# Performance work log

Measured on AMD Instinct MI355X. Metric: run time of the kernel, lower is better.

## Reference

```python
import jax, jax.numpy as jnp
import numpy as np

N_NODES = 100000
N_EDGES = 1600000
IN_DIM, HID_DIM, OUT_DIM = 128, 64, 64


def setup_inputs() -> dict:
    key = jax.random.key(0)
    ks = jax.random.split(key, 6)
    feat = jax.random.normal(ks[0], (N_NODES, IN_DIM), dtype=jnp.float32)
    W1 = jax.random.normal(ks[1], (IN_DIM, HID_DIM), dtype=jnp.float32) * (IN_DIM ** -0.5)
    W2 = jax.random.normal(ks[2], (HID_DIM, HID_DIM), dtype=jnp.float32) * (HID_DIM ** -0.5)
    W3 = jax.random.normal(ks[3], (HID_DIM, OUT_DIM), dtype=jnp.float32) * (HID_DIM ** -0.5)
    b1 = jnp.zeros((HID_DIM,), jnp.float32)
    b2 = jnp.zeros((HID_DIM,), jnp.float32)
    b3 = jnp.zeros((OUT_DIM,), jnp.float32)
    src = jax.random.randint(ks[4], (N_EDGES,), 0, N_NODES, dtype=jnp.int32)
    dst = jax.random.randint(ks[5], (N_EDGES,), 0, N_NODES, dtype=jnp.int32)
    return {"feat": feat, "W1": W1, "b1": b1, "W2": W2, "b2": b2,
            "W3": W3, "b3": b3, "src": src, "dst": dst}


def _degree_norms(src, dst, n_nodes):
    ones = jnp.ones(src.shape[0], jnp.float32)
    out_deg = jax.ops.segment_sum(ones, src, num_segments=n_nodes)
    in_deg = jax.ops.segment_sum(ones, dst, num_segments=n_nodes)
    # DGL GraphConv norm='both': D_out^{-1/2} on source side, D_in^{-1/2} on dest side
    norm_src = jnp.clip(out_deg, 1.0, None) ** -0.5
    norm_dst = jnp.clip(in_deg, 1.0, None) ** -0.5
    return norm_src, norm_dst


def _graph_conv(h, W, b, src, dst, norm_src, norm_dst, n_nodes):
    # mult-first (in_dim >= out_dim path of DGL; linear so mathematically equivalent)
    hw = (h * norm_src[:, None]) @ W          # [N, out]
    msgs = hw[src]                             # [E, out] gather
    agg = jax.ops.segment_sum(msgs, dst, num_segments=n_nodes)  # [N, out] scatter-add
    return agg * norm_dst[:, None] + b


def reference(feat, W1, b1, W2, b2, W3, b3, src, dst):
    n_nodes = feat.shape[0]
    norm_src, norm_dst = _degree_norms(src, dst, n_nodes)
    h = feat
    for W, b in ((W1, b1), (W2, b2), (W3, b3)):
        h = _graph_conv(h, W, b, src, dst, norm_src, norm_dst, n_nodes)
        h = jax.nn.relu(h)
    return h
```

## Files before the change

### kernel.cpp

```cpp
#include <hip/hip_runtime.h>
#include <hip/hip_fp16.h>
#include <type_traits>

#define N_NODES 100000
#define N_EDGES 1600000
#define NB 391
#define CHUNKS 128
#define EPB (N_EDGES / CHUNKS)
#define HALF_NODES 50000
#define WORDS_HALF 12500
#define WORDS_ALL 25000

__global__ void __launch_bounds__(256) hist_kernel(const int* __restrict__ src,
                                                   const int* __restrict__ dst,
                                                   unsigned* __restrict__ histA,
                                                   unsigned* __restrict__ histB) {
    __shared__ unsigned h[WORDS_HALF];
    const int b   = blockIdx.x;
    const int dir = b >> 8;
    const int r   = (b >> 7) & 1;
    const int c   = b & 127;
    const int* __restrict__ ids = dir ? dst : src;
    unsigned* __restrict__ hist = dir ? histB : histA;
    for (int i = threadIdx.x; i < WORDS_HALF; i += 256) h[i] = 0u;
    __syncthreads();
    const int base = c * EPB;
    const int lo   = r * HALF_NODES;
    for (int e = base + threadIdx.x; e < base + EPB; e += 256) {
        int id = ids[e] - lo;
        if ((unsigned)id < (unsigned)HALF_NODES)
            atomicAdd(&h[id >> 2], 1u << ((id & 3) * 8));
    }
    __syncthreads();
    unsigned* __restrict__ out = hist + c * WORDS_ALL + r * WORDS_HALF;
    for (int i = threadIdx.x; i < WORDS_HALF; i += 256) out[i] = h[i];
}

__global__ void reduce_src_kernel(const unsigned* __restrict__ histA,
                                  float* __restrict__ norm_src) {
    const int w = blockIdx.x * 256 + threadIdx.x;
    if (w >= WORDS_ALL) return;
    unsigned s0 = 0, s1 = 0, s2 = 0, s3 = 0;
#pragma unroll 4
    for (int c = 0; c < CHUNKS; ++c) {
        unsigned v = histA[c * WORDS_ALL + w];
        s0 += v & 255u;
        s1 += (v >> 8) & 255u;
        s2 += (v >> 16) & 255u;
        s3 += v >> 24;
    }
    const int n = w * 4;
    norm_src[n + 0] = rsqrtf((float)(s0 > 1u ? s0 : 1u));
    norm_src[n + 1] = rsqrtf((float)(s1 > 1u ? s1 : 1u));
    norm_src[n + 2] = rsqrtf((float)(s2 > 1u ? s2 : 1u));
    norm_src[n + 3] = rsqrtf((float)(s3 > 1u ? s3 : 1u));
}

__global__ void scan_dst_kernel(unsigned* __restrict__ histB,
                                unsigned* __restrict__ ideg,
                                float* __restrict__ norm_dst) {
    const int w = blockIdx.x * 256 + threadIdx.x;
    if (w >= WORDS_ALL) return;
    unsigned run = 0;
#pragma unroll 4
    for (int c = 0; c < CHUNKS; ++c) {
        unsigned v = histB[c * WORDS_ALL + w];
        histB[c * WORDS_ALL + w] = run;
        run += v;
    }
    unsigned s0 = run & 255u, s1 = (run >> 8) & 255u, s2 = (run >> 16) & 255u, s3 = run >> 24;
    const int n = w * 4;
    ideg[n + 0] = s0; ideg[n + 1] = s1; ideg[n + 2] = s2; ideg[n + 3] = s3;
    norm_dst[n + 0] = rsqrtf((float)(s0 > 1u ? s0 : 1u));
    norm_dst[n + 1] = rsqrtf((float)(s1 > 1u ? s1 : 1u));
    norm_dst[n + 2] = rsqrtf((float)(s2 > 1u ? s2 : 1u));
    norm_dst[n + 3] = rsqrtf((float)(s3 > 1u ? s3 : 1u));
}

__global__ void partial_sum_kernel(const unsigned* __restrict__ ideg, int* __restrict__ blocksum) {
    __shared__ int s[256];
    int i = blockIdx.x * 256 + threadIdx.x;
    int c = (i < N_NODES) ? (int)ideg[i] : 0;
    s[threadIdx.x] = c;
    __syncthreads();
    for (int off = 128; off > 0; off >>= 1) {
        if (threadIdx.x < off) s[threadIdx.x] += s[threadIdx.x + off];
        __syncthreads();
    }
    if (threadIdx.x == 0) blocksum[blockIdx.x] = s[0];
}

__global__ void scan_sums_kernel(const int* __restrict__ blocksum, int* __restrict__ blockoff,
                                 int* __restrict__ row_start) {
    __shared__ int s[512];
    const int t = threadIdx.x;
    int v0 = (t < NB) ? blocksum[t] : 0;
    s[t] = v0;
    __syncthreads();
    for (int off = 1; off < 512; off <<= 1) {
        int v = (t >= off) ? s[t - off] : 0;
        __syncthreads();
        s[t] += v;
        __syncthreads();
    }
    if (t < NB) blockoff[t] = s[t] - v0;
    if (t == 0) row_start[N_NODES] = N_EDGES;
}

__global__ void write_offsets_kernel(const unsigned* __restrict__ ideg, const int* __restrict__ blockoff,
                                     int* __restrict__ row_start) {
    __shared__ int s[256];
    const int t = threadIdx.x;
    const int i = blockIdx.x * 256 + t;
    int c = (i < N_NODES) ? (int)ideg[i] : 0;
    s[t] = c;
    __syncthreads();
    for (int off = 1; off < 256; off <<= 1) {
        int v = (t >= off) ? s[t - off] : 0;
        __syncthreads();
        s[t] += v;
        __syncthreads();
    }
    if (i < N_NODES) row_start[i] = blockoff[blockIdx.x] + s[t] - c;
}

__global__ void __launch_bounds__(256) scatter_kernel(const int* __restrict__ src,
                                                      const int* __restrict__ dst,
                                                      const unsigned* __restrict__ histB,
                                                      const int* __restrict__ row_start,
                                                      int* __restrict__ sorted_src) {
    __shared__ unsigned cur[WORDS_HALF];
    const int c = blockIdx.x;
    const int r = blockIdx.y;
    const unsigned* __restrict__ pref = histB + c * WORDS_ALL + r * WORDS_HALF;
    for (int i = threadIdx.x; i < WORDS_HALF; i += 256) cur[i] = pref[i];
    __syncthreads();
    const int base = c * EPB;
    const int lo   = r * HALF_NODES;
    for (int e = base + threadIdx.x; e < base + EPB; e += 256) {
        int d  = dst[e];
        int dl = d - lo;
        if ((unsigned)dl < (unsigned)HALF_NODES) {
            unsigned old = atomicAdd(&cur[dl >> 2], 1u << ((dl & 3) * 8));
            unsigned rk  = (old >> ((dl & 3) * 8)) & 255u;
            sorted_src[row_start[d] + (int)rk] = src[e];
        }
    }
}

template <int K, typename IN>
__global__ void __launch_bounds__(256) gemm_kernel(const IN* __restrict__ h,
                                                   const float* __restrict__ W,
                                                   const float* __restrict__ norm_src,
                                                   __half* __restrict__ out) {
    __shared__ float Ws[K * 64];
    __shared__ float hs[64][68];
    const int t  = threadIdx.x;
    const int ty = t >> 4;
    const int tx = t & 15;
    const int nb = blockIdx.x * 64;

#pragma unroll
    for (int i = 0; i < K * 16 / 256; ++i)
        ((float4*)Ws)[i * 256 + t] = ((const float4*)W)[i * 256 + t];

    float a[4][4];
#pragma unroll
    for (int m = 0; m < 4; ++m)
#pragma unroll
        for (int j = 0; j < 4; ++j) a[m][j] = 0.f;

    for (int kk = 0; kk < K; kk += 64) {
        __syncthreads();
        if constexpr (std::is_same<IN, float>::value) {
#pragma unroll
            for (int r = 0; r < 4; ++r) {
                int e = r * 1024 + t * 4;
                int m = e >> 6, k = e & 63;
                int node = nb + m;
                float4 v = make_float4(0.f, 0.f, 0.f, 0.f);
                if (node < N_NODES) v = *(const float4*)&h[(size_t)node * K + kk + k];
                *(float4*)&hs[m][k] = v;
            }
        } else {
#pragma unroll
            for (int r = 0; r < 2; ++r) {
                int e = r * 2048 + t * 8;
                int m = e >> 6, k = e & 63;
                int node = nb + m;
                float4 lo = make_float4(0.f, 0.f, 0.f, 0.f);
                float4 hi = make_float4(0.f, 0.f, 0.f, 0.f);
                if (node < N_NODES) {
                    uint4 raw = *reinterpret_cast<const uint4*>(&h[(size_t)node * K + kk + k]);
                    float2 f0 = __half22float2(*reinterpret_cast<__half2*>(&raw.x));
                    float2 f1 = __half22float2(*reinterpret_cast<__half2*>(&raw.y));
                    float2 f2 = __half22float2(*reinterpret_cast<__half2*>(&raw.z));
                    float2 f3 = __half22float2(*reinterpret_cast<__half2*>(&raw.w));
                    lo = make_float4(f0.x, f0.y, f1.x, f1.y);
                    hi = make_float4(f2.x, f2.y, f3.x, f3.y);
                }
                *(float4*)&hs[m][k]     = lo;
                *(float4*)&hs[m][k + 4] = hi;
            }
        }
        __syncthreads();

#pragma unroll 4
        for (int k = 0; k < 64; k += 4) {
            float w[4][4], hr[4][4];
#pragma unroll
            for (int i = 0; i < 4; ++i) {
                float4 wv = *(const float4*)&Ws[(kk + k + i) * 64 + tx * 4];
                w[i][0] = wv.x; w[i][1] = wv.y; w[i][2] = wv.z; w[i][3] = wv.w;
            }
#pragma unroll
            for (int m = 0; m < 4; ++m) {
                float4 hv = *(const float4*)&hs[ty * 4 + m][k];
                hr[m][0] = hv.x; hr[m][1] = hv.y; hr[m][2] = hv.z; hr[m][3] = hv.w;
            }
#pragma unroll
            for (int m = 0; m < 4; ++m)
#pragma unroll
                for (int i = 0; i < 4; ++i)
#pragma unroll
                    for (int j = 0; j < 4; ++j)
                        a[m][j] = fmaf(hr[m][i], w[i][j], a[m][j]);
        }
    }

#pragma unroll
    for (int m = 0; m < 4; ++m) {
        int node = nb + ty * 4 + m;
        if (node < N_NODES) {
            float ns = norm_src[node];
            __half2 p0 = __floats2half2_rn(a[m][0] * ns, a[m][1] * ns);
            __half2 p1 = __floats2half2_rn(a[m][2] * ns, a[m][3] * ns);
            uint2 raw;
            raw.x = *reinterpret_cast<unsigned*>(&p0);
            raw.y = *reinterpret_cast<unsigned*>(&p1);
            *reinterpret_cast<uint2*>(&out[(size_t)node * 64 + tx * 4]) = raw;
        }
    }
}

template <typename OUT>
__global__ void __launch_bounds__(256) agg_kernel(const __half* __restrict__ hw,
                                                  const int* __restrict__ sorted_src,
                                                  const int* __restrict__ row_start,
                                                  const float* __restrict__ norm_dst,
                                                  const float* __restrict__ b,
                                                  OUT* __restrict__ out) {
    const int node = blockIdx.x * 4 + (threadIdx.x >> 6);
    const int lane = threadIdx.x & 63;
    const int g    = lane >> 3;
    const int q    = lane & 7;
    const int beg = row_start[node];
    const int end = row_start[node + 1];

    float a0[8], a1[8], a2[8], a3[8];
#pragma unroll
    for (int j = 0; j < 8; ++j) { a0[j] = 0.f; a1[j] = 0.f; a2[j] = 0.f; a3[j] = 0.f; }

#define GCN_GATHER(acc, idx)                                                                  \
    do {                                                                                      \
        uint4 raw = *reinterpret_cast<const uint4*>(&hw[(size_t)sorted_src[idx] * 64 + q * 8]); \
        float2 f0 = __half22float2(*reinterpret_cast<__half2*>(&raw.x));                      \
        float2 f1 = __half22float2(*reinterpret_cast<__half2*>(&raw.y));                      \
        float2 f2 = __half22float2(*reinterpret_cast<__half2*>(&raw.z));                      \
        float2 f3 = __half22float2(*reinterpret_cast<__half2*>(&raw.w));                      \
        acc[0] += f0.x; acc[1] += f0.y; acc[2] += f1.x; acc[3] += f1.y;                       \
        acc[4] += f2.x; acc[5] += f2.y; acc[6] += f3.x; acc[7] += f3.y;                       \
    } while (0)

    for (int e = beg + g; e < end; e += 32) {
        int i0 = e, i1 = e + 8, i2 = e + 16, i3 = e + 24;
        if (i0 < end) GCN_GATHER(a0, i0);
        if (i1 < end) GCN_GATHER(a1, i1);
        if (i2 < end) GCN_GATHER(a2, i2);
        if (i3 < end) GCN_GATHER(a3, i3);
    }
#undef GCN_GATHER

#pragma unroll
    for (int j = 0; j < 8; ++j) a0[j] += a1[j] + a2[j] + a3[j];

#pragma unroll
    for (int j = 0; j < 8; ++j) {
        a0[j] += __shfl_xor(a0[j], 8);
        a0[j] += __shfl_xor(a0[j], 16);
        a0[j] += __shfl_xor(a0[j], 32);
    }

    if (g == 0) {
        float ns = norm_dst[node];
        float o[8];
#pragma unroll
        for (int j = 0; j < 8; ++j) {
            float v = fmaf(a0[j], ns, b[q * 8 + j]);
            o[j] = v > 0.f ? v : 0.f;
        }
        if constexpr (std::is_same<OUT, float>::value) {
            *(float4*)&out[(size_t)node * 64 + q * 8]     = make_float4(o[0], o[1], o[2], o[3]);
            *(float4*)&out[(size_t)node * 64 + q * 8 + 4] = make_float4(o[4], o[5], o[6], o[7]);
        } else {
            __half2 p0 = __floats2half2_rn(o[0], o[1]);
            __half2 p1 = __floats2half2_rn(o[2], o[3]);
            __half2 p2 = __floats2half2_rn(o[4], o[5]);
            __half2 p3 = __floats2half2_rn(o[6], o[7]);
            uint4 raw;
            raw.x = *reinterpret_cast<unsigned*>(&p0);
            raw.y = *reinterpret_cast<unsigned*>(&p1);
            raw.z = *reinterpret_cast<unsigned*>(&p2);
            raw.w = *reinterpret_cast<unsigned*>(&p3);
            *reinterpret_cast<uint4*>(&out[(size_t)node * 64 + q * 8]) = raw;
        }
    }
}

extern "C" void kernel_launch(void* const* d_in, const int* in_sizes, int n_in,
                              void* d_out, int out_size, void* d_ws, size_t ws_size,
                              hipStream_t stream) {
    const float* feat = (const float*)d_in[0];
    const float* W1   = (const float*)d_in[1];
    const float* b1   = (const float*)d_in[2];
    const float* W2   = (const float*)d_in[3];
    const float* b2   = (const float*)d_in[4];
    const float* W3   = (const float*)d_in[5];
    const float* b3   = (const float*)d_in[6];
    const int*   src  = (const int*)d_in[7];
    const int*   dst  = (const int*)d_in[8];
    float* out = (float*)d_out;

    char* ws = (char*)d_ws;
    size_t off = 0;
    auto alloc = [&](size_t bytes) { char* p = ws + off; off += (bytes + 255) & ~size_t(255); return p; };
    float*    norm_src   = (float*)alloc(N_NODES * 4);
    float*    norm_dst   = (float*)alloc(N_NODES * 4);
    unsigned* ideg       = (unsigned*)alloc(N_NODES * 4);
    int*      row_start  = (int*)alloc((N_NODES + 1) * 4);
    int*      blocksum   = (int*)alloc(NB * 4);
    int*      blockoff   = (int*)alloc(NB * 4);
    int*      sorted_src = (int*)alloc(N_EDGES * 4);
    __half*   hw         = (__half*)alloc(N_NODES * 64 * 2);
    __half*   hb         = (__half*)alloc(N_NODES * 64 * 2);

    unsigned* histA = (unsigned*)hw;
    unsigned* histB = (unsigned*)hb;

    hist_kernel<<<512, 256, 0, stream>>>(src, dst, histA, histB);
    reduce_src_kernel<<<98, 256, 0, stream>>>(histA, norm_src);
    scan_dst_kernel<<<98, 256, 0, stream>>>(histB, ideg, norm_dst);

    partial_sum_kernel<<<NB, 256, 0, stream>>>(ideg, blocksum);
    scan_sums_kernel<<<1, 512, 0, stream>>>(blocksum, blockoff, row_start);
    write_offsets_kernel<<<NB, 256, 0, stream>>>(ideg, blockoff, row_start);

    scatter_kernel<<<dim3(128, 2), 256, 0, stream>>>(src, dst, histB, row_start, sorted_src);

    const int GEMM_GRID = (N_NODES + 63) / 64;
    const int AGG_GRID  = (N_NODES + 3) / 4;

    gemm_kernel<128, float><<<GEMM_GRID, 256, 0, stream>>>(feat, W1, norm_src, hw);
    agg_kernel<__half><<<AGG_GRID, 256, 0, stream>>>(hw, sorted_src, row_start, norm_dst, b1, hb);

    gemm_kernel<64, __half><<<GEMM_GRID, 256, 0, stream>>>(hb, W2, norm_src, hw);
    agg_kernel<__half><<<AGG_GRID, 256, 0, stream>>>(hw, sorted_src, row_start, norm_dst, b2, hb);

    gemm_kernel<64, __half><<<GEMM_GRID, 256, 0, stream>>>(hb, W3, norm_src, hw);
    agg_kernel<float><<<AGG_GRID, 256, 0, stream>>>(hw, sorted_src, row_start, norm_dst, b3, out);
}
```

Baseline: 381.8 us.

## Fuse degree/partial-sum kernels, vectorise offsets, and use half-wave per node in aggregation

Merges the source-degree reduction, destination scan and block partial sums into one kernel, shrinking the block-sum scan to 98 blocks. Offsets and histogram init/copy are vectorised to 4 words per thread. The aggregation kernel now assigns 32 lanes per node instead of 64 with a single accumulator set, which should raise lane utilisation at the average degree of 16. In exchange, each group carries less memory-level parallelism per lane.

```diff
diff --git a/kernel.cpp b/kernel.cpp
--- a/kernel.cpp
+++ b/kernel.cpp
@@ -4,25 +4,27 @@
 
 #define N_NODES 100000
 #define N_EDGES 1600000
-#define NB 391
 #define CHUNKS 128
 #define EPB (N_EDGES / CHUNKS)
 #define HALF_NODES 50000
 #define WORDS_HALF 12500
 #define WORDS_ALL 25000
+#define VEC_HALF 3125
+#define NBB 98
 
 __global__ void __launch_bounds__(256) hist_kernel(const int* __restrict__ src,
                                                    const int* __restrict__ dst,
                                                    unsigned* __restrict__ histA,
                                                    unsigned* __restrict__ histB) {
-    __shared__ unsigned h[WORDS_HALF];
+    __shared__ __align__(16) unsigned h[WORDS_HALF];
     const int b   = blockIdx.x;
     const int dir = b >> 8;
     const int r   = (b >> 7) & 1;
     const int c   = b & 127;
     const int* __restrict__ ids = dir ? dst : src;
     unsigned* __restrict__ hist = dir ? histB : histA;
-    for (int i = threadIdx.x; i < WORDS_HALF; i += 256) h[i] = 0u;
+    for (int i = threadIdx.x; i < VEC_HALF; i += 256)
+        ((uint4*)h)[i] = make_uint4(0u, 0u, 0u, 0u);
     __syncthreads();
     const int base = c * EPB;
     const int lo   = r * HALF_NODES;
@@ -32,88 +34,91 @@
             atomicAdd(&h[id >> 2], 1u << ((id & 3) * 8));
     }
     __syncthreads();
-    unsigned* __restrict__ out = hist + c * WORDS_ALL + r * WORDS_HALF;
-    for (int i = threadIdx.x; i < WORDS_HALF; i += 256) out[i] = h[i];
-}
-
-__global__ void reduce_src_kernel(const unsigned* __restrict__ histA,
-                                  float* __restrict__ norm_src) {
-    const int w = blockIdx.x * 256 + threadIdx.x;
-    if (w >= WORDS_ALL) return;
-    unsigned s0 = 0, s1 = 0, s2 = 0, s3 = 0;
+    unsigned* __restrict__ outp = hist + c * WORDS_ALL + r * WORDS_HALF;
+    for (int i = threadIdx.x; i < VEC_HALF; i += 256)
+        ((uint4*)outp)[i] = ((const uint4*)h)[i];
+}
+
+__global__ void __launch_bounds__(256) degrees_kernel(const unsigned* __restrict__ histA,
+                                                      unsigned* __restrict__ histB,
+                                                      float* __restrict__ norm_src,
+                                                      unsigned* __restrict__ ideg,
+                                                      float* __restrict__ norm_dst,
+                                                      int* __restrict__ blocksum) {
+    __shared__ int sred[256];
+    const int t = threadIdx.x;
+    const int w = blockIdx.x * 256 + t;
+    if (blockIdx.y == 0) {
+        if (w >= WORDS_ALL) return;
+        unsigned s0 = 0, s1 = 0, s2 = 0, s3 = 0;
 #pragma unroll 4
-    for (int c = 0; c < CHUNKS; ++c) {
-        unsigned v = histA[c * WORDS_ALL + w];
-        s0 += v & 255u;
-        s1 += (v >> 8) & 255u;
-        s2 += (v >> 16) & 255u;
-        s3 += v >> 24;
-    }
-    const int n = w * 4;
-    norm_src[n + 0] = rsqrtf((float)(s0 > 1u ? s0 : 1u));
-    norm_src[n + 1] = rsqrtf((float)(s1 > 1u ? s1 : 1u));
-    norm_src[n + 2] = rsqrtf((float)(s2 > 1u ? s2 : 1u));
-    norm_src[n + 3] = rsqrtf((float)(s3 > 1u ? s3 : 1u));
-}
-
-__global__ void scan_dst_kernel(unsigned* __restrict__ histB,
-                                unsigned* __restrict__ ideg,
-                                float* __restrict__ norm_dst) {
-    const int w = blockIdx.x * 256 + threadIdx.x;
-    if (w >= WORDS_ALL) return;
-    unsigned run = 0;
+        for (int c = 0; c < CHUNKS; ++c) {
+            unsigned v = histA[c * WORDS_ALL + w];
+            s0 += v & 255u; s1 += (v >> 8) & 255u; s2 += (v >> 16) & 255u; s3 += v >> 24;
+        }
+        const int n = w * 4;
+        norm_src[n + 0] = rsqrtf((float)(s0 > 1u ? s0 : 1u));
+        norm_src[n + 1] = rsqrtf((float)(s1 > 1u ? s1 : 1u));
+        norm_src[n + 2] = rsqrtf((float)(s2 > 1u ? s2 : 1u));
+        norm_src[n + 3] = rsqrtf((float)(s3 > 1u ? s3 : 1u));
+    } else {
+        unsigned s0 = 0, s1 = 0, s2 = 0, s3 = 0;
+        if (w < WORDS_ALL) {
+            unsigned run = 0;
 #pragma unroll 4
-    for (int c = 0; c < CHUNKS; ++c) {
-        unsigned v = histB[c * WORDS_ALL + w];
-        histB[c * WORDS_ALL + w] = run;
-        run += v;
-    }
-    unsigned s0 = run & 255u, s1 = (run >> 8) & 255u, s2 = (run >> 16) & 255u, s3 = run >> 24;
-    const int n = w * 4;
-    ideg[n + 0] = s0; ideg[n + 1] = s1; ideg[n + 2] = s2; ideg[n + 3] = s3;
-    norm_dst[n + 0] = rsqrtf((float)(s0 > 1u ? s0 : 1u));
-    norm_dst[n + 1] = rsqrtf((float)(s1 > 1u ? s1 : 1u));
-    norm_dst[n + 2] = rsqrtf((float)(s2 > 1u ? s2 : 1u));
-    norm_dst[n + 3] = rsqrtf((float)(s3 > 1u ? s3 : 1u));
-}
-
-__global__ void partial_sum_kernel(const unsigned* __restrict__ ideg, int* __restrict__ blocksum) {
-    __shared__ int s[256];
-    int i = blockIdx.x * 256 + threadIdx.x;
-    int c = (i < N_NODES) ? (int)ideg[i] : 0;
-    s[threadIdx.x] = c;
-    __syncthreads();
-    for (int off = 128; off > 0; off >>= 1) {
-        if (threadIdx.x < off) s[threadIdx.x] += s[threadIdx.x + off];
-        __syncthreads();
-    }
-    if (threadIdx.x == 0) blocksum[blockIdx.x] = s[0];
+            for (int c = 0; c < CHUNKS; ++c) {
+                unsigned v = histB[c * WORDS_ALL + w];
+                histB[c * WORDS_ALL + w] = run;
+                run += v;
+            }
+            s0 = run & 255u; s1 = (run >> 8) & 255u; s2 = (run >> 16) & 255u; s3 = run >> 24;
+            const int n = w * 4;
+            ideg[n + 0] = s0; ideg[n + 1] = s1; ideg[n + 2] = s2; ideg[n + 3] = s3;
+            norm_dst[n + 0] = rsqrtf((float)(s0 > 1u ? s0 : 1u));
+            norm_dst[n + 1] = rsqrtf((float)(s1 > 1u ? s1 : 1u));
+            norm_dst[n + 2] = rsqrtf((float)(s2 > 1u ? s2 : 1u));
+            norm_dst[n + 3] = rsqrtf((float)(s3 > 1u ? s3 : 1u));
+        }
+        sred[t] = (int)(s0 + s1 + s2 + s3);
+        __syncthreads();
+        for (int off = 128; off > 0; off >>= 1) {
+            if (t < off) sred[t] += sred[t + off];
+            __syncthreads();
+        }
+        if (t == 0) blocksum[blockIdx.x] = sred[0];
+    }
 }
 
 __global__ void scan_sums_kernel(const int* __restrict__ blocksum, int* __restrict__ blockoff,
                                  int* __restrict__ row_start) {
-    __shared__ int s[512];
+    __shared__ int s[128];
     const int t = threadIdx.x;
-    int v0 = (t < NB) ? blocksum[t] : 0;
+    int v0 = (t < NBB) ? blocksum[t] : 0;
     s[t] = v0;
     __syncthreads();
-    for (int off = 1; off < 512; off <<= 1) {
+    for (int off = 1; off < 128; off <<= 1) {
         int v = (t >= off) ? s[t - off] : 0;
         __syncthreads();
         s[t] += v;
         __syncthreads();
     }
-    if (t < NB) blockoff[t] = s[t] - v0;
+    if (t < NBB) blockoff[t] = s[t] - v0;
     if (t == 0) row_start[N_NODES] = N_EDGES;
 }
 
-__global__ void write_offsets_kernel(const unsigned* __restrict__ ideg, const int* __restrict__ blockoff,
-                                     int* __restrict__ row_start) {
+__global__ void __launch_bounds__(256) write_offsets_kernel(const unsigned* __restrict__ ideg,
+                                                            const int* __restrict__ blockoff,
+                                                            int* __restrict__ row_start) {
     __shared__ int s[256];
     const int t = threadIdx.x;
-    const int i = blockIdx.x * 256 + t;
-    int c = (i < N_NODES) ? (int)ideg[i] : 0;
-    s[t] = c;
+    const int w = blockIdx.x * 256 + t;
+    unsigned c0 = 0, c1 = 0, c2 = 0, c3 = 0;
+    if (w < WORDS_ALL) {
+        uint4 v = *(const uint4*)&ideg[w * 4];
+        c0 = v.x; c1 = v.y; c2 = v.z; c3 = v.w;
+    }
+    int tot = (int)(c0 + c1 + c2 + c3);
+    s[t] = tot;
     __syncthreads();
     for (int off = 1; off < 256; off <<= 1) {
         int v = (t >= off) ? s[t - off] : 0;
@@ -121,7 +126,15 @@
         s[t] += v;
         __syncthreads();
     }
-    if (i < N_NODES) row_start[i] = blockoff[blockIdx.x] + s[t] - c;
+    if (w < WORDS_ALL) {
+        int e = blockoff[blockIdx.x] + s[t] - tot;
+        int4 o;
+        o.x = e;
+        o.y = e + (int)c0;
+        o.z = e + (int)(c0 + c1);
+        o.w = e + (int)(c0 + c1 + c2);
+        *(int4*)&row_start[w * 4] = o;
+    }
 }
 
 __global__ void __launch_bounds__(256) scatter_kernel(const int* __restrict__ src,
@@ -129,11 +142,12 @@
                                                       const unsigned* __restrict__ histB,
                                                       const int* __restrict__ row_start,
                                                       int* __restrict__ sorted_src) {
-    __shared__ unsigned cur[WORDS_HALF];
+    __shared__ __align__(16) unsigned cur[WORDS_HALF];
     const int c = blockIdx.x;
     const int r = blockIdx.y;
     const unsigned* __restrict__ pref = histB + c * WORDS_ALL + r * WORDS_HALF;
-    for (int i = threadIdx.x; i < WORDS_HALF; i += 256) cur[i] = pref[i];
+    for (int i = threadIdx.x; i < VEC_HALF; i += 256)
+        ((uint4*)cur)[i] = ((const uint4*)pref)[i];
     __syncthreads();
     const int base = c * EPB;
     const int lo   = r * HALF_NODES;
@@ -250,45 +264,41 @@
                                                   const float* __restrict__ norm_dst,
                                                   const float* __restrict__ b,
                                                   OUT* __restrict__ out) {
-    const int node = blockIdx.x * 4 + (threadIdx.x >> 6);
-    const int lane = threadIdx.x & 63;
-    const int g    = lane >> 3;
-    const int q    = lane & 7;
+    const int node = blockIdx.x * 8 + (threadIdx.x >> 5);
+    const int l32  = threadIdx.x & 31;
+    const int g    = l32 >> 3;
+    const int q    = l32 & 7;
     const int beg = row_start[node];
     const int end = row_start[node + 1];
 
-    float a0[8], a1[8], a2[8], a3[8];
-#pragma unroll
-    for (int j = 0; j < 8; ++j) { a0[j] = 0.f; a1[j] = 0.f; a2[j] = 0.f; a3[j] = 0.f; }
-
-#define GCN_GATHER(acc, idx)                                                                  \
+    float a[8];
+#pragma unroll
+    for (int j = 0; j < 8; ++j) a[j] = 0.f;
+
+#define GCN_GATHER(idx)                                                                       \
     do {                                                                                      \
         uint4 raw = *reinterpret_cast<const uint4*>(&hw[(size_t)sorted_src[idx] * 64 + q * 8]); \
         float2 f0 = __half22float2(*reinterpret_cast<__half2*>(&raw.x));                      \
         float2 f1 = __half22float2(*reinterpret_cast<__half2*>(&raw.y));                      \
         float2 f2 = __half22float2(*reinterpret_cast<__half2*>(&raw.z));                      \
         float2 f3 = __half22float2(*reinterpret_cast<__half2*>(&raw.w));                      \
-        acc[0] += f0.x; acc[1] += f0.y; acc[2] += f1.x; acc[3] += f1.y;                       \
-        acc[4] += f2.x; acc[5] += f2.y; acc[6] += f3.x; acc[7] += f3.y;                       \
+        a[0] += f0.x; a[1] += f0.y; a[2] += f1.x; a[3] += f1.y;                               \
+        a[4] += f2.x; a[5] += f2.y; a[6] += f3.x; a[7] += f3.y;                               \
     } while (0)
 
-    for (int e = beg + g; e < end; e += 32) {
-        int i0 = e, i1 = e + 8, i2 = e + 16, i3 = e + 24;
-        if (i0 < end) GCN_GATHER(a0, i0);
-        if (i1 < end) GCN_GATHER(a1, i1);
-        if (i2 < end) GCN_GATHER(a2, i2);
-        if (i3 < end) GCN_GATHER(a3, i3);
+    for (int e = beg + g; e < end; e += 16) {
+        int i1 = e + 4, i2 = e + 8, i3 = e + 12;
+        GCN_GATHER(e);
+        if (i1 < end) GCN_GATHER(i1);
+        if (i2 < end) GCN_GATHER(i2);
+        if (i3 < end) GCN_GATHER(i3);
     }
 #undef GCN_GATHER
 
 #pragma unroll
-    for (int j = 0; j < 8; ++j) a0[j] += a1[j] + a2[j] + a3[j];
-
-#pragma unroll
     for (int j = 0; j < 8; ++j) {
-        a0[j] += __shfl_xor(a0[j], 8);
-        a0[j] += __shfl_xor(a0[j], 16);
-        a0[j] += __shfl_xor(a0[j], 32);
+        a[j] += __shfl_xor(a[j], 8);
+        a[j] += __shfl_xor(a[j], 16);
     }
 
     if (g == 0) {
@@ -296,7 +306,7 @@
         float o[8];
 #pragma unroll
         for (int j = 0; j < 8; ++j) {
-            float v = fmaf(a0[j], ns, b[q * 8 + j]);
+            float v = fmaf(a[j], ns, b[q * 8 + j]);
             o[j] = v > 0.f ? v : 0.f;
         }
         if constexpr (std::is_same<OUT, float>::value) {
@@ -338,8 +348,8 @@
     float*    norm_dst   = (float*)alloc(N_NODES * 4);
     unsigned* ideg       = (unsigned*)alloc(N_NODES * 4);
     int*      row_start  = (int*)alloc((N_NODES + 1) * 4);
-    int*      blocksum   = (int*)alloc(NB * 4);
-    int*      blockoff   = (int*)alloc(NB * 4);
+    int*      blocksum   = (int*)alloc(NBB * 4);
+    int*      blockoff   = (int*)alloc(NBB * 4);
     int*      sorted_src = (int*)alloc(N_EDGES * 4);
     __half*   hw         = (__half*)alloc(N_NODES * 64 * 2);
     __half*   hb         = (__half*)alloc(N_NODES * 64 * 2);
@@ -348,17 +358,15 @@
     unsigned* histB = (unsigned*)hb;
 
     hist_kernel<<<512, 256, 0, stream>>>(src, dst, histA, histB);
-    reduce_src_kernel<<<98, 256, 0, stream>>>(histA, norm_src);
-    scan_dst_kernel<<<98, 256, 0, stream>>>(histB, ideg, norm_dst);
-
-    partial_sum_kernel<<<NB, 256, 0, stream>>>(ideg, blocksum);
-    scan_sums_kernel<<<1, 512, 0, stream>>>(blocksum, blockoff, row_start);
-    write_offsets_kernel<<<NB, 256, 0, stream>>>(ideg, blockoff, row_start);
+    degrees_kernel<<<dim3(NBB, 2), 256, 0, stream>>>(histA, histB, norm_src, ideg, norm_dst, blocksum);
+
+    scan_sums_kernel<<<1, 128, 0, stream>>>(blocksum, blockoff, row_start);
+    write_offsets_kernel<<<NBB, 256, 0, stream>>>(ideg, blockoff, row_start);
 
     scatter_kernel<<<dim3(128, 2), 256, 0, stream>>>(src, dst, histB, row_start, sorted_src);
 
     const int GEMM_GRID = (N_NODES + 63) / 64;
-    const int AGG_GRID  = (N_NODES + 3) / 4;
+    const int AGG_GRID  = N_NODES / 8;
 
     gemm_kernel<128, float><<<GEMM_GRID, 256, 0, stream>>>(feat, W1, norm_src, hw);
     agg_kernel<__half><<<AGG_GRID, 256, 0, stream>>>(hw, sorted_src, row_start, norm_dst, b1, hb);
```

Result: faster. 355.8 us (-6.8%).
